# Kernel optimization log

Hardware: AMD Instinct MI355X
Metric: run time of the kernel (lower is better)

Reference implementation:

```python
import jax, jax.numpy as jnp
import numpy as np

B, S, D = 4, 2048, 1024
H = 16            # n_heads
HD = D // H       # head_dim = 64
F = 64            # feature_dim of linear-attention feature map


def setup_inputs() -> dict:
    key = jax.random.key(0)
    ks = jax.random.split(key, 16)
    w = lambda k, shape: jax.random.normal(k, shape, dtype=jnp.float32) * 0.02
    return {
        "x": jax.random.normal(ks[0], (B, S, D), dtype=jnp.float32),
        # flash-attention branch params (Linear stored as [in, out])
        "fq": w(ks[1], (D, D)),
        "fk": w(ks[2], (D, D)),
        "fv": w(ks[3], (D, D)),
        "fo_w": w(ks[4], (D, D)),
        "fo_b": jnp.zeros((D,), jnp.float32),
        # linear-attention branch params
        "lq": w(ks[5], (D, D)),
        "lk": w(ks[6], (D, D)),
        "lv": w(ks[7], (D, D)),
        "lo_w": w(ks[8], (D, D)),
        "lo_b": jnp.zeros((D,), jnp.float32),
        "fm_w": w(ks[9], (HD, F)),
        "fm_b": jnp.zeros((F,), jnp.float32),
        # gate
        "gate_w": w(ks[10], (D, 1)),
        "gate_b": jnp.zeros((1,), jnp.float32),
    }


def reference(x, fq, fk, fv, fo_w, fo_b, lq, lk, lv, lo_w, lo_b,
              fm_w, fm_b, gate_w, gate_b):
    b, s, d = x.shape
    # ---- flash (standard softmax) attention path ----
    q = (x @ fq).reshape(b, s, H, HD)
    k = (x @ fk).reshape(b, s, H, HD)
    v = (x @ fv).reshape(b, s, H, HD)
    scale = 1.0 / np.sqrt(HD).astype(np.float32)
    scores = jnp.einsum('bqhd,bkhd->bhqk', q, k) * scale
    attn = jax.nn.softmax(scores, axis=-1)
    flash = jnp.einsum('bhqk,bkhd->bqhd', attn, v).reshape(b, s, d)
    flash_out = flash @ fo_w + fo_b
    # ---- linear (kernelized) attention path ----
    ql = (x @ lq).reshape(b, s, H, HD)
    kl = (x @ lk).reshape(b, s, H, HD)
    vl = (x @ lv).reshape(b, s, H, HD)
    qf = jax.nn.relu(ql @ fm_w + fm_b)   # [b,s,h,f]
    kf = jax.nn.relu(kl @ fm_w + fm_b)
    kv = jnp.einsum('blhf,blhd->bhfd', kf, vl)
    lin = jnp.einsum('blhf,bhfd->blhd', qf, kv)
    k_sum = kf.sum(axis=1)                               # [b,h,f]
    norm = jnp.einsum('blhf,bhf->blh', qf, k_sum)[..., None]
    lin = lin / jnp.maximum(norm, 1e-6)
    linear_out = lin.reshape(b, s, d) @ lo_w + lo_b
    # ---- sigmoid gate blend ----
    gate = jax.nn.sigmoid(x @ gate_w + gate_b)           # [b,s,1]
    return gate * flash_out + (1.0 - gate) * linear_out
```

## Files before the change

### kernel.cpp

```cpp
#include <hip/hip_runtime.h>
#include <math.h>

typedef __attribute__((ext_vector_type(4))) float f32x4;
typedef __attribute__((ext_vector_type(16))) float f32x16;
typedef __attribute__((ext_vector_type(8))) short s16x8;
typedef __attribute__((ext_vector_type(8))) unsigned short u16x8;

constexpr int Bc = 4, Sc = 2048, Dc = 1024, Hc = 16, HDc = 64, Fc = 64;
constexpr int Rc = Bc * Sc;
constexpr size_t MAT = (size_t)Rc * Dc;
constexpr int KST = 88;
constexpr int NCH = 16;

__device__ __forceinline__ float bf2f(unsigned short u) {
    union { unsigned int i; float f; } v; v.i = ((unsigned int)u) << 16; return v.f;
}
__device__ __forceinline__ unsigned short f2bf(float f) {
    union { float f; unsigned int i; } v; v.f = f;
    unsigned int r = v.i + 0x7FFFu + ((v.i >> 16) & 1u);
    return (unsigned short)(r >> 16);
}
__device__ __forceinline__ unsigned cvtpk(float a, float b) {
    unsigned r;
    asm("v_cvt_pk_bf16_f32 %0, %1, %2" : "=v"(r) : "v"(a), "v"(b));
    return r;
}
__device__ __forceinline__ void async16(const void* g, void* l) {
    __builtin_amdgcn_global_load_lds(
        (const __attribute__((address_space(1))) unsigned int*)g,
        (__attribute__((address_space(3))) unsigned int*)l, 16, 0, 0);
}

__global__ __launch_bounds__(256) void gate_cvt(const float* __restrict__ x,
        const float* __restrict__ gw, const float* __restrict__ gb,
        float* __restrict__ G, unsigned short* __restrict__ Y) {
    const int lane = threadIdx.x & 63;
    const int wave = threadIdx.x >> 6;
    const int r = blockIdx.x * 4 + wave;
    const size_t base = (size_t)r * Dc;
    float acc = 0.f;
    #pragma unroll
    for (int i = 0; i < 4; ++i) {
        int off = (lane + 64 * i) * 4;
        float4 v = *(const float4*)(x + base + off);
        float4 w = *(const float4*)(gw + off);
        acc += v.x * w.x + v.y * w.y + v.z * w.z + v.w * w.w;
        ushort4 o;
        o.x = f2bf(v.x); o.y = f2bf(v.y); o.z = f2bf(v.z); o.w = f2bf(v.w);
        *(ushort4*)(Y + base + off) = o;
    }
    #pragma unroll
    for (int off = 32; off > 0; off >>= 1) acc += __shfl_down(acc, off, 64);
    if (lane == 0) {
        float z = acc + gb[0];
        G[r] = 1.f / (1.f + __expf(-z));
    }
}

__global__ __launch_bounds__(256) void wtrans(
        const float* W0, const float* W1, const float* W2, const float* W3,
        const float* W4, const float* W5, const float* W6, const float* W7,
        unsigned short* T0, unsigned short* T1, unsigned short* T2, unsigned short* T3,
        unsigned short* T4, unsigned short* T5, unsigned short* T6, unsigned short* T7) {
    const float* W; unsigned short* T;
    switch (blockIdx.z) {
        case 0: W = W0; T = T0; break;  case 1: W = W1; T = T1; break;
        case 2: W = W2; T = T2; break;  case 3: W = W3; T = T3; break;
        case 4: W = W4; T = T4; break;  case 5: W = W5; T = T5; break;
        case 6: W = W6; T = T6; break;  default: W = W7; T = T7; break;
    }
    __shared__ float tile[64][65];
    const int t = threadIdx.x;
    const int r0 = blockIdx.x * 64, c0 = blockIdx.y * 64;
    #pragma unroll
    for (int i = 0; i < 4; ++i) {
        int row = (t >> 4) + 16 * i, col = (t & 15) * 4;
        float4 v = *(const float4*)(W + (size_t)(r0 + row) * 1024 + c0 + col);
        tile[row][col] = v.x; tile[row][col + 1] = v.y;
        tile[row][col + 2] = v.z; tile[row][col + 3] = v.w;
    }
    __syncthreads();
    #pragma unroll
    for (int i = 0; i < 4; ++i) {
        int orow = (t >> 4) + 16 * i, ocol = (t & 15) * 4;
        ushort4 o;
        o.x = f2bf(tile[ocol][orow]);     o.y = f2bf(tile[ocol + 1][orow]);
        o.z = f2bf(tile[ocol + 2][orow]); o.w = f2bf(tile[ocol + 3][orow]);
        *(ushort4*)(T + (size_t)(c0 + orow) * 1024 + r0 + ocol) = o;
    }
}

__global__ __launch_bounds__(256) void w2build(const unsigned short* __restrict__ WTq,
        const unsigned short* __restrict__ WTk, const float* __restrict__ fmw,
        unsigned short* __restrict__ W2q, unsigned short* __restrict__ W2k) {
    const int h = blockIdx.x, kc = blockIdx.y, mat = blockIdx.z;
    const unsigned short* WTin = mat ? WTk : WTq;
    unsigned short* W2out = mat ? W2k : W2q;
    __shared__ float Wf[64][65];
    __shared__ float Ws[64][129];
    const int tid = threadIdx.x;
    #pragma unroll
    for (int i = 0; i < 4; ++i) {
        int idx = tid + 256 * i;
        int d = idx >> 4, c4 = (idx & 15) * 4;
        float4 v = *(const float4*)(fmw + d * 64 + c4);
        Wf[d][c4] = v.x; Wf[d][c4 + 1] = v.y; Wf[d][c4 + 2] = v.z; Wf[d][c4 + 3] = v.w;
    }
    #pragma unroll
    for (int i = 0; i < 4; ++i) {
        int idx = tid + 256 * i;
        int d = idx >> 4, c8 = (idx & 15) * 8;
        u16x8 v = *(const u16x8*)(WTin + (size_t)(h * 64 + d) * 1024 + kc * 128 + c8);
        #pragma unroll
        for (int j = 0; j < 8; ++j) Ws[d][c8 + j] = bf2f(v[j]);
    }
    __syncthreads();
    const int f = tid & 63, kw = tid >> 6;
    float acc[32];
    #pragma unroll
    for (int i = 0; i < 32; ++i) acc[i] = 0.f;
    for (int d = 0; d < 64; ++d) {
        float wf = Wf[d][f];
        #pragma unroll
        for (int i = 0; i < 32; ++i) acc[i] += wf * Ws[d][kw + 4 * i];
    }
    unsigned short* orow = W2out + (size_t)(h * 64 + f) * 1024 + kc * 128;
    #pragma unroll
    for (int i = 0; i < 32; ++i) orow[kw + 4 * i] = f2bf(acc[i]);
}

__global__ __launch_bounds__(256) void gemm3(const unsigned short* __restrict__ A,
        const unsigned short* __restrict__ WTa, const unsigned short* __restrict__ WTb,
        unsigned short* __restrict__ C0, unsigned short* __restrict__ C1,
        unsigned short* __restrict__ C2, const float* __restrict__ fmb) {
    __shared__ unsigned short As[128 * 32];
    __shared__ unsigned short Bs[128 * 32];
    const int tid = threadIdx.x, wave = tid >> 6, lane = tid & 63;
    const int lid = blockIdx.x + 64 * blockIdx.y;
    const int xcd = lid & 7, seq = lid >> 3;
    const int rp = 8 * xcd + (seq & 7);
    const int cp = seq >> 3;
    const int brow = rp * 128;
    unsigned short* C = (cp < 8) ? C0 : (cp < 16 ? C1 : C2);
    const int bcol = (cp & 7) * 128;
    const unsigned short* WT = (cp < 16) ? (WTa + (size_t)cp * 128 * 1024)
                                         : (WTb + (size_t)(cp - 16) * 128 * 1024);
    const bool doRelu = (fmb != nullptr) && (cp < 16);
    const int wm = wave >> 1, wn = wave & 1;
    const int lr = lane & 15, g8 = (lane >> 4) * 8;
    const int srow = 32 * wave + (lane >> 2);
    const int scol = (lane & 3) * 8;
    f32x4 acc[4][4];
    #pragma unroll
    for (int m = 0; m < 4; ++m)
        #pragma unroll
        for (int n = 0; n < 4; ++n) acc[m][n] = (f32x4){0.f, 0.f, 0.f, 0.f};
    for (int k0 = 0; k0 < 1024; k0 += 32) {
        __syncthreads();
        #pragma unroll
        for (int i = 0; i < 2; ++i) {
            async16(A  + (size_t)(brow + srow + 16 * i) * 1024 + k0 + scol, &As[(32 * wave + 16 * i) * 32]);
            async16(WT + (size_t)(srow + 16 * i) * 1024 + k0 + scol, &Bs[(32 * wave + 16 * i) * 32]);
        }
        __syncthreads();
        s16x8 af[4], bf[4];
        #pragma unroll
        for (int m = 0; m < 4; ++m) af[m] = *(const s16x8*)&As[(64 * wm + 16 * m + lr) * 32 + g8];
        #pragma unroll
        for (int n = 0; n < 4; ++n) bf[n] = *(const s16x8*)&Bs[(64 * wn + 16 * n + lr) * 32 + g8];
        #pragma unroll
        for (int m = 0; m < 4; ++m)
            #pragma unroll
            for (int n = 0; n < 4; ++n)
                acc[m][n] = __builtin_amdgcn_mfma_f32_16x16x32_bf16(af[m], bf[n], acc[m][n], 0, 0, 0);
    }
    const int rg = (lane >> 4) * 4;
    #pragma unroll
    for (int m = 0; m < 4; ++m)
        #pragma unroll
        for (int n = 0; n < 4; ++n) {
            float bias = doRelu ? fmb[16 * n + lr] : 0.f;
            #pragma unroll
            for (int j = 0; j < 4; ++j) {
                float v = acc[m][n][j];
                if (doRelu) v = fmaxf(v + bias, 0.f);
                C[(size_t)(brow + 64 * wm + 16 * m + rg + j) * 1024 + bcol + 64 * wn + 16 * n + lr] =
                    f2bf(v);
            }
        }
}

__global__ __launch_bounds__(256) void final_gemm(const unsigned short* __restrict__ A1,
        const unsigned short* __restrict__ WT1, const unsigned short* __restrict__ A2,
        const unsigned short* __restrict__ WT2, const float* __restrict__ b1,
        const float* __restrict__ b2, const float* __restrict__ G, float* __restrict__ OUT) {
    __shared__ unsigned short As[128 * 32];
    __shared__ unsigned short Bs[128 * 32];
    const int tid = threadIdx.x, wave = tid >> 6, lane = tid & 63;
    const int lid = blockIdx.x + 64 * blockIdx.y;
    const int xcd = lid & 7, seq = lid >> 3;
    const int brow = (8 * xcd + (seq & 7)) * 128;
    const int bcol = (seq >> 3) * 128;
    const int wm = wave >> 1, wn = wave & 1;
    const int lr = lane & 15, g8 = (lane >> 4) * 8;
    const int srow = 32 * wave + (lane >> 2);
    const int scol = (lane & 3) * 8;
    f32x4 acc[4][4];
    #pragma unroll
    for (int m = 0; m < 4; ++m)
        #pragma unroll
        for (int n = 0; n < 4; ++n) acc[m][n] = (f32x4){0.f, 0.f, 0.f, 0.f};
    for (int pass = 0; pass < 2; ++pass) {
        const unsigned short* A  = pass ? A2 : A1;
        const unsigned short* WT = pass ? WT2 : WT1;
        for (int k0 = 0; k0 < 1024; k0 += 32) {
            __syncthreads();
            #pragma unroll
            for (int i = 0; i < 2; ++i) {
                async16(A  + (size_t)(brow + srow + 16 * i) * 1024 + k0 + scol, &As[(32 * wave + 16 * i) * 32]);
                async16(WT + (size_t)(bcol + srow + 16 * i) * 1024 + k0 + scol, &Bs[(32 * wave + 16 * i) * 32]);
            }
            __syncthreads();
            s16x8 af[4], bf[4];
            #pragma unroll
            for (int m = 0; m < 4; ++m) af[m] = *(const s16x8*)&As[(64 * wm + 16 * m + lr) * 32 + g8];
            #pragma unroll
            for (int n = 0; n < 4; ++n) bf[n] = *(const s16x8*)&Bs[(64 * wn + 16 * n + lr) * 32 + g8];
            #pragma unroll
            for (int m = 0; m < 4; ++m)
                #pragma unroll
                for (int n = 0; n < 4; ++n)
                    acc[m][n] = __builtin_amdgcn_mfma_f32_16x16x32_bf16(af[m], bf[n], acc[m][n], 0, 0, 0);
        }
    }
    const int rg = (lane >> 4) * 4;
    #pragma unroll
    for (int m = 0; m < 4; ++m)
        #pragma unroll
        for (int j = 0; j < 4; ++j) {
            int row = brow + 64 * wm + 16 * m + rg + j;
            float g = G[row];
            #pragma unroll
            for (int n = 0; n < 4; ++n) {
                int col = bcol + 64 * wn + 16 * n + lr;
                OUT[(size_t)row * 1024 + col] = acc[m][n][j] + g * b1[col] + (1.f - g) * b2[col];
            }
        }
}

__global__ __launch_bounds__(512) void flash_mfma(const unsigned short* __restrict__ Qg,
        const unsigned short* __restrict__ Kg, const unsigned short* __restrict__ Vg,
        const float* __restrict__ G, unsigned short* __restrict__ FA) {
    __shared__ unsigned short Ks[2][64 * KST];
    __shared__ unsigned short Vt[2][64 * KST];
    const int tid = threadIdx.x, wave = tid >> 6, lane = tid & 63;
    const int b = blockIdx.x >> 4, h = blockIdx.x & 15, q0 = blockIdx.y * 256;
    const int lq = lane & 31, hi = lane >> 5;
    const float QSCALE = 0.125f * 1.44269504f;
    const size_t qrow = (size_t)b * Sc + q0 + wave * 32 + lq;
    const size_t qoff = qrow * Dc + h * HDc + 8 * hi;
    s16x8 aq[4];
    #pragma unroll
    for (int dc = 0; dc < 4; ++dc) {
        u16x8 raw = *(const u16x8*)(Qg + qoff + 16 * dc);
        #pragma unroll
        for (int j = 0; j < 8; ++j) aq[dc][j] = (short)f2bf(bf2f(raw[j]) * QSCALE);
    }
    const s16x8 ones = {0x3F80, 0x3F80, 0x3F80, 0x3F80, 0x3F80, 0x3F80, 0x3F80, 0x3F80};
    f32x16 oacc[2], lacc;
    #pragma unroll
    for (int t = 0; t < 2; ++t)
        #pragma unroll
        for (int r = 0; r < 16; ++r) oacc[t][r] = 0.f;
    #pragma unroll
    for (int r = 0; r < 16; ++r) lacc[r] = 0.f;
    const int srow = tid >> 3, sc8 = (tid & 7) * 8, va = tid & 7;
    const int p0 = (srow & 3) | (((srow >> 3) & 1) << 2) | (((srow >> 2) & 1) << 3) | (srow & 0x30);
    const int pg = p0 >> 3, pin = p0 & 7;
    const size_t kvoff = (size_t)h * HDc + sc8;
    {
        size_t gg = ((size_t)b * Sc + srow) * Dc + kvoff;
        u16x8 kreg = *(const u16x8*)(Kg + gg);
        u16x8 vreg = *(const u16x8*)(Vg + gg);
        *(u16x8*)&Ks[0][srow * KST + sc8] = kreg;
        #pragma unroll
        for (int j = 0; j < 8; ++j)
            Vt[0][(sc8 + j) * KST + 8 * (pg ^ va) + pin] = vreg[j];
    }
    __syncthreads();
    int cur = 0;
    for (int t0 = 0; t0 < Sc; t0 += 64) {
        const bool nxt = (t0 + 64) < Sc;
        u16x8 kn, vn;
        if (nxt) {
            size_t gg = ((size_t)b * Sc + t0 + 64 + srow) * Dc + kvoff;
            kn = *(const u16x8*)(Kg + gg);
            vn = *(const u16x8*)(Vg + gg);
        }
        f32x16 s2[2];
        #pragma unroll
        for (int t = 0; t < 2; ++t)
            #pragma unroll
            for (int r = 0; r < 16; ++r) s2[t][r] = 0.f;
        __builtin_amdgcn_s_setprio(1);
        #pragma unroll
        for (int kt2 = 0; kt2 < 2; ++kt2)
            #pragma unroll
            for (int dc = 0; dc < 4; ++dc) {
                s16x8 ak = *(const s16x8*)&Ks[cur][(32 * kt2 + lq) * KST + 16 * dc + 8 * hi];
                s2[kt2] = __builtin_amdgcn_mfma_f32_32x32x16_bf16(ak, aq[dc], s2[kt2], 0, 0, 0);
            }
        __builtin_amdgcn_s_setprio(0);
        #pragma unroll
        for (int t = 0; t < 2; ++t)
            #pragma unroll
            for (int r = 0; r < 16; ++r)
                s2[t][r] = exp2f(s2[t][r]);
        s16x8 pf[4];
        #pragma unroll
        for (int kc = 0; kc < 4; ++kc) {
            const int t = kc >> 1, e = 8 * (kc & 1);
            union { s16x8 v; unsigned u[4]; } w;
            w.u[0] = cvtpk(s2[t][e + 0], s2[t][e + 1]);
            w.u[1] = cvtpk(s2[t][e + 2], s2[t][e + 3]);
            w.u[2] = cvtpk(s2[t][e + 4], s2[t][e + 5]);
            w.u[3] = cvtpk(s2[t][e + 6], s2[t][e + 7]);
            pf[kc] = w.v;
        }
        __builtin_amdgcn_s_setprio(1);
        #pragma unroll
        for (int dtile = 0; dtile < 2; ++dtile) {
            const int row = 32 * dtile + lq;
            const int rsw = (row >> 3) & 7;
            #pragma unroll
            for (int kc = 0; kc < 4; ++kc) {
                const int g = 4 * (kc >> 1) + 2 * (kc & 1) + hi;
                s16x8 av = *(const s16x8*)&Vt[cur][row * KST + 8 * (g ^ rsw)];
                oacc[dtile] = __builtin_amdgcn_mfma_f32_32x32x16_bf16(av, pf[kc], oacc[dtile], 0, 0, 0);
            }
        }
        #pragma unroll
        for (int kc = 0; kc < 4; ++kc)
            lacc = __builtin_amdgcn_mfma_f32_32x32x16_bf16(ones, pf[kc], lacc, 0, 0, 0);
        __builtin_amdgcn_s_setprio(0);
        if (nxt) {
            *(u16x8*)&Ks[cur ^ 1][srow * KST + sc8] = kn;
            #pragma unroll
            for (int j = 0; j < 8; ++j)
                Vt[cur ^ 1][(sc8 + j) * KST + 8 * (pg ^ va) + pin] = vn[j];
        }
        __syncthreads();
        cur ^= 1;
    }
    const float scl = G[qrow] / lacc[0];
    #pragma unroll
    for (int dtile = 0; dtile < 2; ++dtile)
        #pragma unroll
        for (int s = 0; s < 4; ++s) {
            ushort4 o4;
            o4.x = f2bf(oacc[dtile][4 * s + 0] * scl);
            o4.y = f2bf(oacc[dtile][4 * s + 1] * scl);
            o4.z = f2bf(oacc[dtile][4 * s + 2] * scl);
            o4.w = f2bf(oacc[dtile][4 * s + 3] * scl);
            *(ushort4*)(FA + qrow * Dc + h * HDc + 32 * dtile + 8 * s + 4 * hi) = o4;
        }
}

__global__ __launch_bounds__(256) void kv_part(const unsigned short* __restrict__ KF,
        const unsigned short* __restrict__ VL, float* __restrict__ PART, float* __restrict__ PARTS) {
    __shared__ float Ks[32][68];
    __shared__ float Vs[32][68];
    const int tid = threadIdx.x;
    const int bh = blockIdx.x;
    const int b = bh >> 4, h = bh & 15;
    const int ch = blockIdx.y;
    const int f = tid >> 2;
    const int dg = (tid & 3) << 4;
    float acc[16] = {};
    float ksum = 0.f;
    const int lbeg = ch * (Sc / NCH), lend = lbeg + Sc / NCH;
    for (int l0 = lbeg; l0 < lend; l0 += 32) {
        __syncthreads();
        for (int i = tid; i < 32 * 64 / 4; i += 256) {
            int r = i >> 4, c = (i & 15) << 2;
            size_t gg = ((size_t)(b * Sc + l0 + r) * Hc + h) * 64 + c;
            ushort4 kk = *(const ushort4*)(KF + gg);
            ushort4 vv = *(const ushort4*)(VL + gg);
            Ks[r][c] = bf2f(kk.x); Ks[r][c + 1] = bf2f(kk.y);
            Ks[r][c + 2] = bf2f(kk.z); Ks[r][c + 3] = bf2f(kk.w);
            Vs[r][c] = bf2f(vv.x); Vs[r][c + 1] = bf2f(vv.y);
            Vs[r][c + 2] = bf2f(vv.z); Vs[r][c + 3] = bf2f(vv.w);
        }
        __syncthreads();
        #pragma unroll 4
        for (int ll = 0; ll < 32; ++ll) {
            float kf = Ks[ll][f];
            ksum += kf;
            float4 v0 = *(const float4*)&Vs[ll][dg];
            float4 v1 = *(const float4*)&Vs[ll][dg + 4];
            float4 v2 = *(const float4*)&Vs[ll][dg + 8];
            float4 v3 = *(const float4*)&Vs[ll][dg + 12];
            acc[0] += kf * v0.x; acc[1] += kf * v0.y; acc[2]  += kf * v0.z; acc[3]  += kf * v0.w;
            acc[4] += kf * v1.x; acc[5] += kf * v1.y; acc[6]  += kf * v1.z; acc[7]  += kf * v1.w;
            acc[8] += kf * v2.x; acc[9] += kf * v2.y; acc[10] += kf * v2.z; acc[11] += kf * v2.w;
            acc[12] += kf * v3.x; acc[13] += kf * v3.y; acc[14] += kf * v3.z; acc[15] += kf * v3.w;
        }
    }
    size_t o = (((size_t)ch * 64 + bh) * 64 + f) * 64 + dg;
    *(float4*)(PART + o)      = make_float4(acc[0], acc[1], acc[2], acc[3]);
    *(float4*)(PART + o + 4)  = make_float4(acc[4], acc[5], acc[6], acc[7]);
    *(float4*)(PART + o + 8)  = make_float4(acc[8], acc[9], acc[10], acc[11]);
    *(float4*)(PART + o + 12) = make_float4(acc[12], acc[13], acc[14], acc[15]);
    if ((tid & 3) == 0) PARTS[((size_t)ch * 64 + bh) * 64 + f] = ksum;
}

__global__ __launch_bounds__(256) void kv_reduce(const float* __restrict__ PART,
        float* __restrict__ KV) {
    size_t i = (size_t)blockIdx.x * 256 + threadIdx.x;
    float s = 0.f;
    #pragma unroll
    for (int ch = 0; ch < NCH; ++ch) s += PART[(size_t)ch * 262144 + i];
    KV[i] = s;
}
__global__ __launch_bounds__(256) void ks_reduce(const float* __restrict__ PARTS,
        float* __restrict__ KS) {
    int i = blockIdx.x * 256 + threadIdx.x;
    float s = 0.f;
    #pragma unroll
    for (int ch = 0; ch < NCH; ++ch) s += PARTS[ch * 4096 + i];
    KS[i] = s;
}

__global__ __launch_bounds__(256) void kvb_build(const float* __restrict__ KV,
        const float* __restrict__ KS, unsigned short* __restrict__ KVB) {
    const int bh = blockIdx.x, t = threadIdx.x;
    for (int i = t; i < 80 * 64; i += 256) {
        int n = i >> 6, f = i & 63;
        float v = (n < 64) ? KV[(size_t)bh * 4096 + f * 64 + n]
                           : (n == 64 ? KS[bh * 64 + f] : 0.f);
        KVB[(size_t)bh * 5120 + i] = f2bf(v);
    }
}

__global__ __launch_bounds__(256) void lin_mfma(const unsigned short* __restrict__ QF,
        const unsigned short* __restrict__ KVB, const float* __restrict__ G,
        unsigned short* __restrict__ LA) {
    __shared__ unsigned short As[128 * 72];
    __shared__ unsigned short Bs[80 * 72];
    const int tid = threadIdx.x, wave = tid >> 6, lane = tid & 63;
    const int bh = blockIdx.y, b = bh >> 4, h = bh & 15;
    const size_t rowg0 = (size_t)b * Sc + blockIdx.x * 128;
    #pragma unroll
    for (int i = 0; i < 4; ++i) {
        int idx = tid + 256 * i;
        int r = idx >> 3, c8 = (idx & 7) * 8;
        *(u16x8*)&As[r * 72 + c8] = *(const u16x8*)(QF + (rowg0 + r) * 1024 + h * 64 + c8);
    }
    #pragma unroll
    for (int i = 0; i < 3; ++i) {
        int idx = tid + 256 * i;
        if (idx < 640) {
            int r = idx >> 3, c8 = (idx & 7) * 8;
            *(u16x8*)&Bs[r * 72 + c8] = *(const u16x8*)(KVB + (size_t)bh * 5120 + r * 64 + c8);
        }
    }
    __syncthreads();
    const int lr = lane & 15, g8 = (lane >> 4) * 8;
    f32x4 acc[2][5];
    #pragma unroll
    for (int m = 0; m < 2; ++m)
        #pragma unroll
        for (int n = 0; n < 5; ++n) acc[m][n] = (f32x4){0.f, 0.f, 0.f, 0.f};
    #pragma unroll
    for (int kc = 0; kc < 2; ++kc) {
        s16x8 af[2];
        #pragma unroll
        for (int m = 0; m < 2; ++m)
            af[m] = *(const s16x8*)&As[(32 * wave + 16 * m + lr) * 72 + kc * 32 + g8];
        #pragma unroll
        for (int n = 0; n < 5; ++n) {
            s16x8 bfv = *(const s16x8*)&Bs[(16 * n + lr) * 72 + kc * 32 + g8];
            #pragma unroll
            for (int m = 0; m < 2; ++m)
                acc[m][n] = __builtin_amdgcn_mfma_f32_16x16x32_bf16(af[m], bfv, acc[m][n], 0, 0, 0);
        }
    }
    const int rg = (lane >> 4) * 4;
    #pragma unroll
    for (int m = 0; m < 2; ++m)
        #pragma unroll
        for (int j = 0; j < 4; ++j) {
            size_t rglob = rowg0 + 32 * wave + 16 * m + rg + j;
            float g = G[rglob];
            float nv = __shfl(acc[m][4][j], lane & 48, 64);
            float inv = (1.f - g) / fmaxf(nv, 1e-6f);
            #pragma unroll
            for (int n = 0; n < 4; ++n)
                LA[rglob * 1024 + h * 64 + 16 * n + lr] = f2bf(acc[m][n][j] * inv);
        }
}

extern "C" void kernel_launch(void* const* d_in, const int* in_sizes, int n_in,
                              void* d_out, int out_size, void* d_ws, size_t ws_size,
                              hipStream_t stream) {
    const float* x   = (const float*)d_in[0];
    const float* fq  = (const float*)d_in[1];
    const float* fk  = (const float*)d_in[2];
    const float* fv  = (const float*)d_in[3];
    const float* fow = (const float*)d_in[4];
    const float* fob = (const float*)d_in[5];
    const float* lq  = (const float*)d_in[6];
    const float* lk  = (const float*)d_in[7];
    const float* lv  = (const float*)d_in[8];
    const float* low = (const float*)d_in[9];
    const float* lob = (const float*)d_in[10];
    const float* fmw = (const float*)d_in[11];
    const float* fmb = (const float*)d_in[12];
    const float* gw  = (const float*)d_in[13];
    const float* gb  = (const float*)d_in[14];
    float* out = (float*)d_out;

    char* p = (char*)d_ws;
    unsigned short* xb = (unsigned short*)p;          p += MAT * 2;
    unsigned short* wt_fq = (unsigned short*)p;       p += (size_t)1024 * 1024 * 2;
    unsigned short* wt_fk = (unsigned short*)p;       p += (size_t)1024 * 1024 * 2;
    unsigned short* wt_fv = (unsigned short*)p;       p += (size_t)1024 * 1024 * 2;
    unsigned short* wt_fo = (unsigned short*)p;       p += (size_t)1024 * 1024 * 2;
    unsigned short* wt_lq = (unsigned short*)p;       p += (size_t)1024 * 1024 * 2;
    unsigned short* wt_lk = (unsigned short*)p;       p += (size_t)1024 * 1024 * 2;
    unsigned short* wt_lv = (unsigned short*)p;       p += (size_t)1024 * 1024 * 2;
    unsigned short* wt_lo = (unsigned short*)p;       p += (size_t)1024 * 1024 * 2;
    unsigned short* P0 = (unsigned short*)p;          p += MAT * 2;
    unsigned short* P1 = (unsigned short*)p;          p += MAT * 2;
    unsigned short* P2 = (unsigned short*)p;          p += MAT * 2;
    unsigned short* FA = (unsigned short*)p;          p += MAT * 2;
    unsigned short* LA = (unsigned short*)p;          p += MAT * 2;
    float* KV = (float*)p;                            p += (size_t)Bc * Hc * Fc * HDc * 4;
    float* KS = (float*)p;                            p += (size_t)Bc * Hc * Fc * 4;
    float* G  = (float*)p;                            p += (size_t)Rc * 4;
    float* PART  = (float*)p;                         p += (size_t)NCH * 64 * 64 * 64 * 4;
    float* PARTS = (float*)p;                         p += (size_t)NCH * 64 * 64 * 4;
    unsigned short* KVB = (unsigned short*)p;         p += (size_t)64 * 80 * 64 * 2;
    unsigned short* W2  = (unsigned short*)p;         p += (size_t)2 * 1024 * 1024 * 2;

    dim3 proj3Grid(Rc / 128, 24);
    dim3 gemmGrid(Rc / 128, Dc / 128);

    gate_cvt<<<Rc / 4, 256, 0, stream>>>(x, gw, gb, G, xb);
    wtrans<<<dim3(16, 16, 8), 256, 0, stream>>>(fq, fk, fv, fow, lq, lk, lv, low,
            wt_fq, wt_fk, wt_fv, wt_fo, wt_lq, wt_lk, wt_lv, wt_lo);
    w2build<<<dim3(16, 8, 2), 256, 0, stream>>>(wt_lq, wt_lk, fmw, W2, W2 + (size_t)1024 * 1024);

    gemm3<<<proj3Grid, 256, 0, stream>>>(xb, W2, wt_lv, P0, P1, P2, fmb);
    kv_part<<<dim3(Bc * Hc, NCH), 256, 0, stream>>>(P1, P2, PART, PARTS);
    kv_reduce<<<(64 * 64 * 64) / 256, 256, 0, stream>>>(PART, KV);
    ks_reduce<<<(64 * 64) / 256, 256, 0, stream>>>(PARTS, KS);
    kvb_build<<<64, 256, 0, stream>>>(KV, KS, KVB);
    lin_mfma<<<dim3(Sc / 128, 64), 256, 0, stream>>>(P0, KVB, G, LA);

    gemm3<<<proj3Grid, 256, 0, stream>>>(xb, wt_fq, wt_fv, P0, P1, P2, nullptr);
    flash_mfma<<<dim3(64, 8), 512, 0, stream>>>(P0, P1, P2, G, FA);

    final_gemm<<<gemmGrid, 256, 0, stream>>>(FA, wt_fo, LA, wt_lo, fob, lob, G, out);
}
```

Baseline: 367.8 us.

## Merge projection GEMMs into one launch, async-load swizzled K tiles, fold KV reductions

Both projection GEMMs now run in a single 48-column-tile launch that writes six outputs. This removes one launch and gives a larger grid for occupancy. The flash kernel loads K tiles through async global-to-LDS copies into an XOR-swizzled unpadded layout instead of going through registers with padding. The separate kv_reduce and ks_reduce kernels are removed by summing the partials directly in kvb_build, at the cost of serial per-element reductions in only 64 blocks.

```diff
diff --git a/kernel.cpp b/kernel.cpp
--- a/kernel.cpp
+++ b/kernel.cpp
@@ -129,23 +129,27 @@
     for (int i = 0; i < 32; ++i) orow[kw + 4 * i] = f2bf(acc[i]);
 }
 
-__global__ __launch_bounds__(256) void gemm3(const unsigned short* __restrict__ A,
-        const unsigned short* __restrict__ WTa, const unsigned short* __restrict__ WTb,
-        unsigned short* __restrict__ C0, unsigned short* __restrict__ C1,
-        unsigned short* __restrict__ C2, const float* __restrict__ fmb) {
+__global__ __launch_bounds__(256) void gemm6(const unsigned short* __restrict__ A,
+        const unsigned short* __restrict__ W2, const unsigned short* __restrict__ WTlv,
+        const unsigned short* __restrict__ WTf,
+        unsigned short* __restrict__ O0, unsigned short* __restrict__ O1,
+        unsigned short* __restrict__ O2, unsigned short* __restrict__ O3,
+        unsigned short* __restrict__ O4, unsigned short* __restrict__ O5,
+        const float* __restrict__ fmb) {
     __shared__ unsigned short As[128 * 32];
     __shared__ unsigned short Bs[128 * 32];
     const int tid = threadIdx.x, wave = tid >> 6, lane = tid & 63;
     const int lid = blockIdx.x + 64 * blockIdx.y;
     const int xcd = lid & 7, seq = lid >> 3;
-    const int rp = 8 * xcd + (seq & 7);
+    const int brow = (8 * xcd + (seq & 7)) * 128;
     const int cp = seq >> 3;
-    const int brow = rp * 128;
-    unsigned short* C = (cp < 8) ? C0 : (cp < 16 ? C1 : C2);
     const int bcol = (cp & 7) * 128;
-    const unsigned short* WT = (cp < 16) ? (WTa + (size_t)cp * 128 * 1024)
-                                         : (WTb + (size_t)(cp - 16) * 128 * 1024);
-    const bool doRelu = (fmb != nullptr) && (cp < 16);
+    const unsigned short* WT;
+    unsigned short* C;
+    bool doRelu = false;
+    if (cp < 16)      { WT = W2 + (size_t)cp * 131072;          C = (cp < 8) ? O0 : O1; doRelu = true; }
+    else if (cp < 24) { WT = WTlv + (size_t)(cp - 16) * 131072; C = O2; }
+    else              { WT = WTf + (size_t)(cp - 24) * 131072;  C = (cp < 32) ? O3 : (cp < 40 ? O4 : O5); }
     const int wm = wave >> 1, wn = wave & 1;
     const int lr = lane & 15, g8 = (lane >> 4) * 8;
     const int srow = 32 * wave + (lane >> 2);
@@ -251,7 +255,7 @@
 __global__ __launch_bounds__(512) void flash_mfma(const unsigned short* __restrict__ Qg,
         const unsigned short* __restrict__ Kg, const unsigned short* __restrict__ Vg,
         const float* __restrict__ G, unsigned short* __restrict__ FA) {
-    __shared__ unsigned short Ks[2][64 * KST];
+    __shared__ unsigned short Ks[2][64 * 64];
     __shared__ unsigned short Vt[2][64 * KST];
     const int tid = threadIdx.x, wave = tid >> 6, lane = tid & 63;
     const int b = blockIdx.x >> 4, h = blockIdx.x & 15, q0 = blockIdx.y * 256;
@@ -274,15 +278,15 @@
         for (int r = 0; r < 16; ++r) oacc[t][r] = 0.f;
     #pragma unroll
     for (int r = 0; r < 16; ++r) lacc[r] = 0.f;
-    const int srow = tid >> 3, sc8 = (tid & 7) * 8, va = tid & 7;
+    const int srow = tid >> 3, gidx = tid & 7, va = tid & 7;
+    const int sc8 = gidx * 8;
+    const int kcol = ((gidx ^ (srow & 7))) * 8;
     const int p0 = (srow & 3) | (((srow >> 3) & 1) << 2) | (((srow >> 2) & 1) << 3) | (srow & 0x30);
     const int pg = p0 >> 3, pin = p0 & 7;
-    const size_t kvoff = (size_t)h * HDc + sc8;
+    async16(Kg + ((size_t)b * Sc + srow) * Dc + h * HDc + kcol, &Ks[0][512 * wave]);
     {
-        size_t gg = ((size_t)b * Sc + srow) * Dc + kvoff;
-        u16x8 kreg = *(const u16x8*)(Kg + gg);
+        size_t gg = ((size_t)b * Sc + srow) * Dc + h * HDc + sc8;
         u16x8 vreg = *(const u16x8*)(Vg + gg);
-        *(u16x8*)&Ks[0][srow * KST + sc8] = kreg;
         #pragma unroll
         for (int j = 0; j < 8; ++j)
             Vt[0][(sc8 + j) * KST + 8 * (pg ^ va) + pin] = vreg[j];
@@ -291,11 +295,11 @@
     int cur = 0;
     for (int t0 = 0; t0 < Sc; t0 += 64) {
         const bool nxt = (t0 + 64) < Sc;
-        u16x8 kn, vn;
+        u16x8 vn;
         if (nxt) {
-            size_t gg = ((size_t)b * Sc + t0 + 64 + srow) * Dc + kvoff;
-            kn = *(const u16x8*)(Kg + gg);
-            vn = *(const u16x8*)(Vg + gg);
+            async16(Kg + ((size_t)b * Sc + t0 + 64 + srow) * Dc + h * HDc + kcol,
+                    &Ks[cur ^ 1][512 * wave]);
+            vn = *(const u16x8*)(Vg + ((size_t)b * Sc + t0 + 64 + srow) * Dc + h * HDc + sc8);
         }
         f32x16 s2[2];
         #pragma unroll
@@ -307,7 +311,8 @@
         for (int kt2 = 0; kt2 < 2; ++kt2)
             #pragma unroll
             for (int dc = 0; dc < 4; ++dc) {
-                s16x8 ak = *(const s16x8*)&Ks[cur][(32 * kt2 + lq) * KST + 16 * dc + 8 * hi];
+                const int row = 32 * kt2 + lq;
+                s16x8 ak = *(const s16x8*)&Ks[cur][row * 64 + 8 * ((2 * dc + hi) ^ (row & 7))];
                 s2[kt2] = __builtin_amdgcn_mfma_f32_32x32x16_bf16(ak, aq[dc], s2[kt2], 0, 0, 0);
             }
         __builtin_amdgcn_s_setprio(0);
@@ -344,7 +349,6 @@
             lacc = __builtin_amdgcn_mfma_f32_32x32x16_bf16(ones, pf[kc], lacc, 0, 0, 0);
         __builtin_amdgcn_s_setprio(0);
         if (nxt) {
-            *(u16x8*)&Ks[cur ^ 1][srow * KST + sc8] = kn;
             #pragma unroll
             for (int j = 0; j < 8; ++j)
                 Vt[cur ^ 1][(sc8 + j) * KST + 8 * (pg ^ va) + pin] = vn[j];
@@ -414,30 +418,21 @@
     if ((tid & 3) == 0) PARTS[((size_t)ch * 64 + bh) * 64 + f] = ksum;
 }
 
-__global__ __launch_bounds__(256) void kv_reduce(const float* __restrict__ PART,
-        float* __restrict__ KV) {
-    size_t i = (size_t)blockIdx.x * 256 + threadIdx.x;
-    float s = 0.f;
-    #pragma unroll
-    for (int ch = 0; ch < NCH; ++ch) s += PART[(size_t)ch * 262144 + i];
-    KV[i] = s;
-}
-__global__ __launch_bounds__(256) void ks_reduce(const float* __restrict__ PARTS,
-        float* __restrict__ KS) {
-    int i = blockIdx.x * 256 + threadIdx.x;
-    float s = 0.f;
-    #pragma unroll
-    for (int ch = 0; ch < NCH; ++ch) s += PARTS[ch * 4096 + i];
-    KS[i] = s;
-}
-
-__global__ __launch_bounds__(256) void kvb_build(const float* __restrict__ KV,
-        const float* __restrict__ KS, unsigned short* __restrict__ KVB) {
+__global__ __launch_bounds__(256) void kvb_build(const float* __restrict__ PART,
+        const float* __restrict__ PARTS, unsigned short* __restrict__ KVB) {
     const int bh = blockIdx.x, t = threadIdx.x;
     for (int i = t; i < 80 * 64; i += 256) {
         int n = i >> 6, f = i & 63;
-        float v = (n < 64) ? KV[(size_t)bh * 4096 + f * 64 + n]
-                           : (n == 64 ? KS[bh * 64 + f] : 0.f);
+        float v = 0.f;
+        if (n < 64) {
+            #pragma unroll
+            for (int ch = 0; ch < NCH; ++ch)
+                v += PART[(size_t)ch * 262144 + (size_t)bh * 4096 + f * 64 + n];
+        } else if (n == 64) {
+            #pragma unroll
+            for (int ch = 0; ch < NCH; ++ch)
+                v += PARTS[(size_t)ch * 4096 + bh * 64 + f];
+        }
         KVB[(size_t)bh * 5120 + i] = f2bf(v);
     }
 }
@@ -533,33 +528,29 @@
     unsigned short* P0 = (unsigned short*)p;          p += MAT * 2;
     unsigned short* P1 = (unsigned short*)p;          p += MAT * 2;
     unsigned short* P2 = (unsigned short*)p;          p += MAT * 2;
-    unsigned short* FA = (unsigned short*)p;          p += MAT * 2;
-    unsigned short* LA = (unsigned short*)p;          p += MAT * 2;
-    float* KV = (float*)p;                            p += (size_t)Bc * Hc * Fc * HDc * 4;
-    float* KS = (float*)p;                            p += (size_t)Bc * Hc * Fc * 4;
+    unsigned short* P3 = (unsigned short*)p;          p += MAT * 2;
+    unsigned short* P4 = (unsigned short*)p;          p += MAT * 2;
+    unsigned short* P5 = (unsigned short*)p;          p += MAT * 2;
     float* G  = (float*)p;                            p += (size_t)Rc * 4;
     float* PART  = (float*)p;                         p += (size_t)NCH * 64 * 64 * 64 * 4;
     float* PARTS = (float*)p;                         p += (size_t)NCH * 64 * 64 * 4;
     unsigned short* KVB = (unsigned short*)p;         p += (size_t)64 * 80 * 64 * 2;
     unsigned short* W2  = (unsigned short*)p;         p += (size_t)2 * 1024 * 1024 * 2;
-
-    dim3 proj3Grid(Rc / 128, 24);
-    dim3 gemmGrid(Rc / 128, Dc / 128);
+    unsigned short* FA = P1;
+    unsigned short* LA = P2;
 
     gate_cvt<<<Rc / 4, 256, 0, stream>>>(x, gw, gb, G, xb);
     wtrans<<<dim3(16, 16, 8), 256, 0, stream>>>(fq, fk, fv, fow, lq, lk, lv, low,
             wt_fq, wt_fk, wt_fv, wt_fo, wt_lq, wt_lk, wt_lv, wt_lo);
     w2build<<<dim3(16, 8, 2), 256, 0, stream>>>(wt_lq, wt_lk, fmw, W2, W2 + (size_t)1024 * 1024);
 
-    gemm3<<<proj3Grid, 256, 0, stream>>>(xb, W2, wt_lv, P0, P1, P2, fmb);
+    gemm6<<<dim3(64, 48), 256, 0, stream>>>(xb, W2, wt_lv, wt_fq, P0, P1, P2, P3, P4, P5, fmb);
+
     kv_part<<<dim3(Bc * Hc, NCH), 256, 0, stream>>>(P1, P2, PART, PARTS);
-    kv_reduce<<<(64 * 64 * 64) / 256, 256, 0, stream>>>(PART, KV);
-    ks_reduce<<<(64 * 64) / 256, 256, 0, stream>>>(PARTS, KS);
-    kvb_build<<<64, 256, 0, stream>>>(KV, KS, KVB);
+    kvb_build<<<64, 256, 0, stream>>>(PART, PARTS, KVB);
     lin_mfma<<<dim3(Sc / 128, 64), 256, 0, stream>>>(P0, KVB, G, LA);
 
-    gemm3<<<proj3Grid, 256, 0, stream>>>(xb, wt_fq, wt_fv, P0, P1, P2, nullptr);
-    flash_mfma<<<dim3(64, 8), 512, 0, stream>>>(P0, P1, P2, G, FA);
-
-    final_gemm<<<gemmGrid, 256, 0, stream>>>(FA, wt_fo, LA, wt_lo, fob, lob, G, out);
-}
+    flash_mfma<<<dim3(64, 8), 512, 0, stream>>>(P3, P4, P5, G, FA);
+
+    final_gemm<<<dim3(64, 8), 256, 0, stream>>>(FA, wt_fo, LA, wt_lo, fob, lob, G, out);
+}
```

Result: slower. 409.3 us (+11.3%).
